# Performance work log

Measured on AMD Instinct MI355X. Metric: run time of the kernel, lower is better.

Reference implementation:

```python
import jax, jax.numpy as jnp
import numpy as np

B, S, E, H = 2, 2048, 1024, 16
D = E // H  # head dim = 64


def setup_inputs() -> dict:
    key = jax.random.key(0)
    ks = jax.random.split(key, 6)
    x = jax.random.normal(ks[0], (B, S, E), dtype=jnp.float32)
    attn_mask = jax.random.bernoulli(ks[1], 0.1, (B, S, S))  # True = masked
    scale = 1.0 / np.sqrt(E)
    w_kernel = jax.random.normal(ks[2], (E, 3 * E), dtype=jnp.float32) * scale
    w_bias = jax.random.normal(ks[3], (3 * E,), dtype=jnp.float32) * 0.02
    fc_kernel = jax.random.normal(ks[4], (E, E), dtype=jnp.float32) * scale
    fc_bias = jax.random.normal(ks[5], (E,), dtype=jnp.float32) * 0.02
    return {"x": x, "attn_mask": attn_mask, "w_kernel": w_kernel,
            "w_bias": w_bias, "fc_kernel": fc_kernel, "fc_bias": fc_bias}


def reference(x, attn_mask, w_kernel, w_bias, fc_kernel, fc_bias):
    b, s, e = x.shape
    qkv = jnp.einsum("bse,ef->bsf", x, w_kernel) + w_bias  # (B,S,3E)
    q, k, v = jnp.split(qkv, 3, axis=-1)

    def heads(t):  # (B,S,E) -> (B,H,S,D)
        return t.reshape(b, s, H, D).transpose(0, 2, 1, 3)

    q, k, v = heads(q), heads(k), heads(v)
    scores = jnp.einsum("bhqd,bhkd->bhqk", q, k) / jnp.sqrt(jnp.float32(D))
    # faithful quirk: masked positions are filled with 1e-9, not -inf
    scores = jnp.where(attn_mask[:, None, :, :], jnp.float32(1e-9), scores)
    A = jax.nn.softmax(scores, axis=-1)
    out = jnp.einsum("bhqk,bhkd->bhqd", A, v)  # (B,H,S,D)
    out = out.transpose(0, 2, 1, 3).reshape(b, s, e)
    # dropout is identity in eval mode
    return jnp.einsum("bse,ef->bsf", out, fc_kernel) + fc_bias
```

## Files before the change

kernel.cpp:

```cpp
#include <hip/hip_runtime.h>
#include <math.h>

#define BB 2
#define SS 2048
#define EE 1024
#define HH 16

typedef _Float16 f16;
typedef __attribute__((ext_vector_type(8))) _Float16 f16x8;
typedef __attribute__((ext_vector_type(4))) _Float16 f16x4;
typedef __attribute__((ext_vector_type(2))) _Float16 f16x2;
typedef __attribute__((ext_vector_type(4))) float f32x4;

union P8 { f16x8 v8; f16x2 h2[4]; };
union V8 { f16x8 v8; f16x4 v4[2]; };

#define QSCALE 0.18033688011112042f

#if __has_builtin(__builtin_amdgcn_exp2f)
#define EXP2(x) __builtin_amdgcn_exp2f(x)
#else
#define EXP2(x) exp2f(x)
#endif

static __device__ __forceinline__ f16x2 pk2(float a, float b) {
#if __has_builtin(__builtin_amdgcn_cvt_pkrtz)
  return __builtin_bit_cast(f16x2, __builtin_amdgcn_cvt_pkrtz(a, b));
#else
  f16x2 r; r[0] = (f16)a; r[1] = (f16)b; return r;
#endif
}

static __device__ __forceinline__ void gl16(const void* g, void* l) {
  __builtin_amdgcn_global_load_lds(
      (const __attribute__((address_space(1))) void*)g,
      (__attribute__((address_space(3))) void*)l, 16, 0, 0);
}

__global__ __launch_bounds__(256) void cvt_f32_f16(
    const float* __restrict__ in, f16* __restrict__ out, int n)
{
  int i = (blockIdx.x * 256 + threadIdx.x) * 8;
  if (i >= n) return;
  float4 a = *(const float4*)(in + i);
  float4 b = *(const float4*)(in + i + 4);
  f16x8 o;
  o[0] = (f16)a.x; o[1] = (f16)a.y; o[2] = (f16)a.z; o[3] = (f16)a.w;
  o[4] = (f16)b.x; o[5] = (f16)b.y; o[6] = (f16)b.z; o[7] = (f16)b.w;
  *(f16x8*)(out + i) = o;
}

__global__ __launch_bounds__(256) void transpose_cvt(
    const float* __restrict__ in, f16* __restrict__ out, int K, int N)
{
  __shared__ float T[64][65];
  const int k0 = blockIdx.y * 64, n0 = blockIdx.x * 64;
  const int tr = threadIdx.x >> 4, tc = (threadIdx.x & 15) * 4;
#pragma unroll
  for (int i = 0; i < 4; ++i) {
    int r = tr + i * 16;
    *(float4*)&T[r][tc] = *(const float4*)(in + (size_t)(k0 + r) * N + n0 + tc);
  }
  __syncthreads();
#pragma unroll
  for (int i = 0; i < 4; ++i) {
    int nl = tr + i * 16;
    f16x4 v;
    v[0] = (f16)T[tc + 0][nl];
    v[1] = (f16)T[tc + 1][nl];
    v[2] = (f16)T[tc + 2][nl];
    v[3] = (f16)T[tc + 3][nl];
    *(f16x4*)(out + (size_t)(n0 + nl) * K + k0 + tc) = v;
  }
}

__global__ __launch_bounds__(256) void pack_mask(
    const int* __restrict__ m, unsigned long long* __restrict__ bits)
{
  const int i = blockIdx.x * 256 + threadIdx.x;
  const unsigned long long bal = __ballot(m[i] != 0);
  if ((threadIdx.x & 63) == 0) bits[i >> 6] = bal;
}

__global__ __launch_bounds__(256) void gemm_f16(
    const f16* __restrict__ A, const f16* __restrict__ Bt,
    const float* __restrict__ bias, int M, int N, int K, int mode,
    f16* __restrict__ oQK, f16* __restrict__ oVT, float* __restrict__ oF32)
{
  __shared__ f16 Ah[128 * 32];
  __shared__ f16 Bh[128 * 32];

  const int t = threadIdx.x;
  const int l = t & 63, w = t >> 6;
  const int l15 = l & 15, l4 = l >> 4;
  const int wr = w >> 1, wc = w & 1;
  const int n0 = blockIdx.x * 128, m0 = blockIdx.y * 128;

  const int srow = l >> 2;
  const int gch  = (l & 3) ^ (srow & 3);
  const f16* Ap0 = A + (size_t)(m0 + w * 32 + srow) * K + gch * 8;
  const f16* Ap1 = Ap0 + (size_t)16 * K;
  const f16* Bp0 = Bt + (size_t)(n0 + w * 32 + srow) * K + gch * 8;
  const f16* Bp1 = Bp0 + (size_t)16 * K;
  f16* ldsA0 = &Ah[(w * 32) * 32];
  f16* ldsA1 = &Ah[(w * 32 + 16) * 32];
  f16* ldsB0 = &Bh[(w * 32) * 32];
  f16* ldsB1 = &Bh[(w * 32 + 16) * 32];

  f32x4 acc[4][4] = {};
  const int csw = (l15 & 3);

  for (int k0 = 0; k0 < K; k0 += 32) {
    gl16(Ap0 + k0, ldsA0);
    gl16(Ap1 + k0, ldsA1);
    gl16(Bp0 + k0, ldsB0);
    gl16(Bp1 + k0, ldsB1);
    __syncthreads();

    f16x8 af[4], bf[4];
#pragma unroll
    for (int mr = 0; mr < 4; ++mr) {
      const int row = wr * 64 + mr * 16 + l15;
      af[mr] = *(const f16x8*)&Ah[row * 32 + ((l4 ^ csw) * 8)];
    }
#pragma unroll
    for (int nr = 0; nr < 4; ++nr) {
      const int row = wc * 64 + nr * 16 + l15;
      bf[nr] = *(const f16x8*)&Bh[row * 32 + ((l4 ^ csw) * 8)];
    }
    __builtin_amdgcn_s_setprio(1);
#pragma unroll
    for (int mr = 0; mr < 4; ++mr)
#pragma unroll
      for (int nr = 0; nr < 4; ++nr)
        acc[mr][nr] = __builtin_amdgcn_mfma_f32_16x16x32_f16(
            af[mr], bf[nr], acc[mr][nr], 0, 0, 0);
    __builtin_amdgcn_s_setprio(0);
    __syncthreads();
  }

  if (mode == 1) {
#pragma unroll
    for (int nr = 0; nr < 4; ++nr) {
      const int n = n0 + wc * 64 + nr * 16 + l15;
      const float bv = bias[n];
#pragma unroll
      for (int mr = 0; mr < 4; ++mr)
#pragma unroll
        for (int j = 0; j < 4; ++j) {
          const int m = m0 + wr * 64 + mr * 16 + l4 * 4 + j;
          oF32[(size_t)m * N + n] = acc[mr][nr][j] + bv;
        }
    }
  } else {
#pragma unroll
    for (int nr = 0; nr < 4; ++nr) {
      const int n = n0 + wc * 64 + nr * 16 + l15;
      const float bv = bias[n];
      if (n < 2048) {
        const float qs = (n < 1024) ? QSCALE : 1.0f;
#pragma unroll
        for (int mr = 0; mr < 4; ++mr)
#pragma unroll
          for (int j = 0; j < 4; ++j) {
            const int m = m0 + wr * 64 + mr * 16 + l4 * 4 + j;
            oQK[(size_t)m * 2048 + n] = (f16)((acc[mr][nr][j] + bv) * qs);
          }
      } else {
        const int hh = (n - 2048) >> 6;
        const int d = (n - 2048) & 63;
#pragma unroll
        for (int mr = 0; mr < 4; ++mr) {
          const int tok0 = m0 + wr * 64 + mr * 16 + l4 * 4;
          const int bq = tok0 >> 11, sq = tok0 & 2047;
          f16x4 v;
          v[0] = (f16)(acc[mr][nr][0] + bv);
          v[1] = (f16)(acc[mr][nr][1] + bv);
          v[2] = (f16)(acc[mr][nr][2] + bv);
          v[3] = (f16)(acc[mr][nr][3] + bv);
          *(f16x4*)(oVT + ((size_t)(bq * 16 + hh) * 64 + d) * SS + sq) = v;
        }
      }
    }
  }
}

#define VPAD 36
__global__ __launch_bounds__(256, 4) void attn_mfma(
    const f16* __restrict__ qkbuf, const f16* __restrict__ vT,
    const unsigned long long* __restrict__ mbits,
    f16* __restrict__ Opart, float* __restrict__ Lpart)
{
  __shared__ f16 Kds[2][32 * 64];
  __shared__ f16 Vds[2][64 * VPAD];

  const int t = threadIdx.x;
  const int w = t >> 6, l = t & 63, l15 = l & 15, l4 = l >> 4;
  const int bh = blockIdx.y, b = bh >> 4, h = bh & 15;
  const int ks = blockIdx.z;
  const int qbase = blockIdx.x * 128 + w * 32;

  f16x8 q00, q01, q10, q11;
  {
    const size_t r0 = (size_t)(b * SS + qbase + l15) * 2048 + h * 64;
    const size_t r1 = (size_t)(b * SS + qbase + 16 + l15) * 2048 + h * 64;
    q00 = *(const f16x8*)(qkbuf + r0 + l4 * 8);
    q01 = *(const f16x8*)(qkbuf + r0 + 32 + l4 * 8);
    q10 = *(const f16x8*)(qkbuf + r1 + l4 * 8);
    q11 = *(const f16x8*)(qkbuf + r1 + 32 + l4 * 8);
  }

  f32x4 accA[4] = {}, accB[4] = {};
  f32x4 accLA = {}, accLB = {};
  f16x8 ones;
#pragma unroll
  for (int i = 0; i < 8; ++i) ones[i] = (f16)1.0f;

  const unsigned int* mA =
      (const unsigned int*)mbits + (size_t)(b * SS + qbase + l15) * 64 + ks * 32;
  const unsigned int* mB =
      (const unsigned int*)mbits + (size_t)(b * SS + qbase + 16 + l15) * 64 + ks * 32;

  const int srow = t >> 3;
  const int scb  = (t & 7) * 8;
  const int sws  = (srow & 7) << 3;
  const f16* kb = qkbuf + (size_t)b * SS * 2048 + 1024 + h * 64 + scb +
                  (size_t)ks * 1024 * 2048;
  const int vd  = t >> 2;
  const int vkb = (t & 3) * 8;
  const f16* vb = vT + ((size_t)bh * 64 + vd) * SS + ks * 1024 + vkb;

  f16x8 kr0; V8 vr0;
#define LOADT(kt)                                                         \
  {                                                                       \
    kr0 = *(const f16x8*)(kb + (size_t)((kt) + srow) * 2048);             \
    vr0.v8 = *(const f16x8*)(vb + (kt));                                  \
  }
#define COMMIT(bi)                                                        \
  {                                                                       \
    *(f16x8*)&Kds[bi][srow * 64 + (scb ^ sws)] = kr0;                     \
    *(f16x4*)&Vds[bi][vd * VPAD + vkb]     = vr0.v4[0];                   \
    *(f16x4*)&Vds[bi][vd * VPAD + vkb + 4] = vr0.v4[1];                   \
  }

  LOADT(0)
  COMMIT(0)
  LOADT(32)
  __syncthreads();

  const int swr = (l15 & 7) << 3;

#define BODY(cur, tI)                                                         \
  {                                                                           \
    const unsigned int mbA = mA[tI];                                          \
    const unsigned int mbB = mB[tI];                                          \
    float pA[8], pB[8];                                                       \
    _Pragma("unroll")                                                         \
    for (int g = 0; g < 2; ++g) {                                             \
      const f16* krow = &Kds[cur][(g * 16 + l15) * 64];                       \
      const f16x8 k0 = *(const f16x8*)(krow + ((l4 * 8) ^ swr));              \
      const f16x8 k1 = *(const f16x8*)(krow + ((32 + l4 * 8) ^ swr));         \
      __builtin_amdgcn_s_setprio(1);                                          \
      f32x4 SA = __builtin_amdgcn_mfma_f32_16x16x32_f16(                      \
          k0, q00, (f32x4){0.f, 0.f, 0.f, 0.f}, 0, 0, 0);                     \
      SA = __builtin_amdgcn_mfma_f32_16x16x32_f16(k1, q01, SA, 0, 0, 0);      \
      f32x4 SB = __builtin_amdgcn_mfma_f32_16x16x32_f16(                      \
          k0, q10, (f32x4){0.f, 0.f, 0.f, 0.f}, 0, 0, 0);                     \
      SB = __builtin_amdgcn_mfma_f32_16x16x32_f16(k1, q11, SB, 0, 0, 0);      \
      __builtin_amdgcn_s_setprio(0);                                          \
      const unsigned int nibA = mbA >> (g * 16 + l4 * 4);                     \
      const unsigned int nibB = mbB >> (g * 16 + l4 * 4);                     \
      _Pragma("unroll")                                                       \
      for (int j = 0; j < 4; ++j) {                                           \
        pA[g * 4 + j] = ((nibA >> j) & 1u) ? 1.0f : EXP2(SA[j]);              \
        pB[g * 4 + j] = ((nibB >> j) & 1u) ? 1.0f : EXP2(SB[j]);              \
      }                                                                       \
    }                                                                         \
    P8 uA, uB;                                                                \
    uA.h2[0] = pk2(pA[0], pA[1]); uA.h2[1] = pk2(pA[2], pA[3]);               \
    uA.h2[2] = pk2(pA[4], pA[5]); uA.h2[3] = pk2(pA[6], pA[7]);               \
    uB.h2[0] = pk2(pB[0], pB[1]); uB.h2[1] = pk2(pB[2], pB[3]);               \
    uB.h2[2] = pk2(pB[4], pB[5]); uB.h2[3] = pk2(pB[6], pB[7]);               \
    __builtin_amdgcn_s_setprio(1);                                            \
    _Pragma("unroll")                                                         \
    for (int dg = 0; dg < 4; ++dg) {                                          \
      const f16* vrow = &Vds[cur][(dg * 16 + l15) * VPAD];                    \
      V8 uv;                                                                  \
      uv.v4[0] = *(const f16x4*)(vrow + l4 * 4);                              \
      uv.v4[1] = *(const f16x4*)(vrow + 16 + l4 * 4);                         \
      accA[dg] = __builtin_amdgcn_mfma_f32_16x16x32_f16(uA.v8, uv.v8,         \
                                                        accA[dg], 0, 0, 0);   \
      accB[dg] = __builtin_amdgcn_mfma_f32_16x16x32_f16(uB.v8, uv.v8,         \
                                                        accB[dg], 0, 0, 0);   \
    }                                                                         \
    accLA = __builtin_amdgcn_mfma_f32_16x16x32_f16(uA.v8, ones, accLA,        \
                                                   0, 0, 0);                  \
    accLB = __builtin_amdgcn_mfma_f32_16x16x32_f16(uB.v8, ones, accLB,        \
                                                   0, 0, 0);                  \
    __builtin_amdgcn_s_setprio(0);                                            \
    if ((tI) + 1 < 32) {                                                      \
      COMMIT((cur) ^ 1)                                                       \
      if ((tI) + 2 < 32) LOADT(((tI) + 2) * 32)                               \
    }                                                                         \
    __syncthreads();                                                          \
  }

  for (int tI = 0; tI < 32; tI += 2) {
    BODY(0, tI)
    BODY(1, tI + 1)
  }

  const size_t obase = (size_t)ks * 4096 * EE;
#pragma unroll
  for (int j = 0; j < 4; ++j) {
    const int qr = l4 * 4 + j;
    const size_t rowA = (size_t)(b * SS + qbase + qr) * EE + h * 64 + l15;
    const size_t rowB = (size_t)(b * SS + qbase + 16 + qr) * EE + h * 64 + l15;
#pragma unroll
    for (int dg = 0; dg < 4; ++dg) {
      Opart[obase + rowA + dg * 16] = (f16)accA[dg][j];
      Opart[obase + rowB + dg * 16] = (f16)accB[dg][j];
    }
    if (l15 == 0) {
      Lpart[(size_t)ks * 4096 * HH + (size_t)(b * SS + qbase + qr) * HH + h] =
          accLA[j];
      Lpart[(size_t)ks * 4096 * HH +
            (size_t)(b * SS + qbase + 16 + qr) * HH + h] = accLB[j];
    }
  }
}

__global__ __launch_bounds__(256) void combine(
    const f16* __restrict__ Opart, const float* __restrict__ Lpart,
    f16* __restrict__ aout)
{
  const size_t i = ((size_t)blockIdx.x * 256 + threadIdx.x) * 8;
  const int token = (int)(i >> 10);
  const int h = (int)((i >> 6) & 15);
  const float inv =
      1.0f / (Lpart[(size_t)token * HH + h] +
              Lpart[(size_t)4096 * HH + (size_t)token * HH + h]);
  const f16x8 o0 = *(const f16x8*)(Opart + i);
  const f16x8 o1 = *(const f16x8*)(Opart + (size_t)4096 * EE + i);
  f16x8 o;
#pragma unroll
  for (int j = 0; j < 8; ++j)
    o[j] = (f16)(((float)o0[j] + (float)o1[j]) * inv);
  *(f16x8*)(aout + i) = o;
}

extern "C" void kernel_launch(void* const* d_in, const int* in_sizes, int n_in,
                              void* d_out, int out_size, void* d_ws,
                              size_t ws_size, hipStream_t stream)
{
  (void)in_sizes; (void)n_in; (void)out_size; (void)ws_size;
  const float* x   = (const float*)d_in[0];
  const int* mask  = (const int*)d_in[1];
  const float* wk  = (const float*)d_in[2];
  const float* wb  = (const float*)d_in[3];
  const float* fck = (const float*)d_in[4];
  const float* fcb = (const float*)d_in[5];
  float* out       = (float*)d_out;

  char* ws = (char*)d_ws;
  f16* fckT = (f16*)(ws);
  f16* qk   = (f16*)(ws + 2097152);
  f16* vT   = (f16*)(ws + 18874368);
  unsigned long long* mbits = (unsigned long long*)(ws + 27262976);
  float* Lp = (float*)(ws + 28311552);
  char* scratch = ws + 28835840;
  f16* xh    = (f16*)scratch;
  f16* Wt    = (f16*)(scratch + 8388608);
  f16* Opart = (f16*)scratch;
  f16* aoutH = qk;

  cvt_f32_f16<<<4096 * 1024 / (8 * 256), 256, 0, stream>>>(x, xh, 4096 * 1024);
  transpose_cvt<<<dim3(3072 / 64, 1024 / 64), 256, 0, stream>>>(wk, Wt, 1024, 3072);
  transpose_cvt<<<dim3(1024 / 64, 1024 / 64), 256, 0, stream>>>(fck, fckT, 1024, 1024);
  pack_mask<<<BB * SS * SS / 256, 256, 0, stream>>>(mask, mbits);

  gemm_f16<<<dim3(3072 / 128, 4096 / 128), 256, 0, stream>>>(
      xh, Wt, wb, 4096, 3072, 1024, 0, qk, vT, nullptr);

  attn_mfma<<<dim3(SS / 128, BB * HH, 2), 256, 0, stream>>>(
      qk, vT, mbits, Opart, Lp);
  combine<<<4096 * 1024 / (8 * 256), 256, 0, stream>>>(Opart, Lp, aoutH);

  gemm_f16<<<dim3(1024 / 128, 4096 / 128), 256, 0, stream>>>(
      aoutH, fckT, fcb, 4096, 1024, 1024, 1, nullptr, nullptr, out);
}
```

Before: 243.3 us.

## Merge prep kernels, stage QK epilogue through LDS, retile FC GEMM

Folds the four preprocessing kernels (x conversion, two weight transposes, mask packing) into a single launch that splits the work by block index, removing three launches. The QKV GEMM is specialised and its Q/K epilogue now goes through swizzled shared memory so each row is written with wide 16-byte stores instead of scattered 2-byte ones. The output-projection GEMM uses 128x64 tiles to double the block count and improve occupancy on the smaller N=1024 problem. The extra LDS round-trip and syncs add some epilogue cost.

```diff
diff --git a/kernel.cpp b/kernel.cpp
--- a/kernel.cpp
+++ b/kernel.cpp
@@ -37,58 +37,75 @@
       (__attribute__((address_space(3))) void*)l, 16, 0, 0);
 }
 
-__global__ __launch_bounds__(256) void cvt_f32_f16(
-    const float* __restrict__ in, f16* __restrict__ out, int n)
-{
-  int i = (blockIdx.x * 256 + threadIdx.x) * 8;
-  if (i >= n) return;
-  float4 a = *(const float4*)(in + i);
-  float4 b = *(const float4*)(in + i + 4);
-  f16x8 o;
-  o[0] = (f16)a.x; o[1] = (f16)a.y; o[2] = (f16)a.z; o[3] = (f16)a.w;
-  o[4] = (f16)b.x; o[5] = (f16)b.y; o[6] = (f16)b.z; o[7] = (f16)b.w;
-  *(f16x8*)(out + i) = o;
-}
-
-__global__ __launch_bounds__(256) void transpose_cvt(
-    const float* __restrict__ in, f16* __restrict__ out, int K, int N)
-{
+__global__ __launch_bounds__(256) void prep(
+    const float* __restrict__ x, f16* __restrict__ xh,
+    const float* __restrict__ wk, f16* __restrict__ Wt,
+    const float* __restrict__ fck, f16* __restrict__ fckT,
+    const int* __restrict__ mask, unsigned long long* __restrict__ mbits)
+{
+  const int bid = blockIdx.x;
+  const int tid = threadIdx.x;
   __shared__ float T[64][65];
-  const int k0 = blockIdx.y * 64, n0 = blockIdx.x * 64;
-  const int tr = threadIdx.x >> 4, tc = (threadIdx.x & 15) * 4;
-#pragma unroll
-  for (int i = 0; i < 4; ++i) {
-    int r = tr + i * 16;
-    *(float4*)&T[r][tc] = *(const float4*)(in + (size_t)(k0 + r) * N + n0 + tc);
-  }
-  __syncthreads();
-#pragma unroll
-  for (int i = 0; i < 4; ++i) {
-    int nl = tr + i * 16;
-    f16x4 v;
-    v[0] = (f16)T[tc + 0][nl];
-    v[1] = (f16)T[tc + 1][nl];
-    v[2] = (f16)T[tc + 2][nl];
-    v[3] = (f16)T[tc + 3][nl];
-    *(f16x4*)(out + (size_t)(n0 + nl) * K + k0 + tc) = v;
-  }
-}
-
-__global__ __launch_bounds__(256) void pack_mask(
-    const int* __restrict__ m, unsigned long long* __restrict__ bits)
-{
-  const int i = blockIdx.x * 256 + threadIdx.x;
-  const unsigned long long bal = __ballot(m[i] != 0);
-  if ((threadIdx.x & 63) == 0) bits[i >> 6] = bal;
-}
-
-__global__ __launch_bounds__(256) void gemm_f16(
+
+  if (bid < 2048) {
+    const int i = (bid * 256 + tid) * 8;
+    float4 a = *(const float4*)(x + i);
+    float4 b = *(const float4*)(x + i + 4);
+    f16x8 o;
+    o[0] = (f16)a.x; o[1] = (f16)a.y; o[2] = (f16)a.z; o[3] = (f16)a.w;
+    o[4] = (f16)b.x; o[5] = (f16)b.y; o[6] = (f16)b.z; o[7] = (f16)b.w;
+    *(f16x8*)(xh + i) = o;
+    return;
+  }
+  if (bid < 3072) {
+    const float* in; f16* outp; int K, N, bx, by;
+    if (bid < 2816) {
+      const int lb = bid - 2048;
+      bx = lb % 48; by = lb / 48; in = wk; outp = Wt; K = 1024; N = 3072;
+    } else {
+      const int lb = bid - 2816;
+      bx = lb & 15; by = lb >> 4; in = fck; outp = fckT; K = 1024; N = 1024;
+    }
+    const int k0 = by * 64, n0 = bx * 64;
+    const int tr = tid >> 4, tc = (tid & 15) * 4;
+#pragma unroll
+    for (int i = 0; i < 4; ++i) {
+      int r = tr + i * 16;
+      *(float4*)&T[r][tc] = *(const float4*)(in + (size_t)(k0 + r) * N + n0 + tc);
+    }
+    __syncthreads();
+#pragma unroll
+    for (int i = 0; i < 4; ++i) {
+      int nl = tr + i * 16;
+      f16x4 v;
+      v[0] = (f16)T[tc + 0][nl];
+      v[1] = (f16)T[tc + 1][nl];
+      v[2] = (f16)T[tc + 2][nl];
+      v[3] = (f16)T[tc + 3][nl];
+      *(f16x4*)(outp + (size_t)(n0 + nl) * K + k0 + tc) = v;
+    }
+    return;
+  }
+  const int lb = bid - 3072;
+  const int wg = lb * 4 + (tid >> 6);
+  const int lane = tid & 63;
+  const size_t base = (size_t)wg * 256;
+#pragma unroll
+  for (int k = 0; k < 4; ++k) {
+    const unsigned long long bal = __ballot(mask[base + k * 64 + lane] != 0);
+    if (lane == 0) mbits[(base >> 6) + k] = bal;
+  }
+}
+
+__global__ __launch_bounds__(256) void gemm_qkv(
     const f16* __restrict__ A, const f16* __restrict__ Bt,
-    const float* __restrict__ bias, int M, int N, int K, int mode,
-    f16* __restrict__ oQK, f16* __restrict__ oVT, float* __restrict__ oF32)
-{
-  __shared__ f16 Ah[128 * 32];
-  __shared__ f16 Bh[128 * 32];
+    const float* __restrict__ bias,
+    f16* __restrict__ oQK, f16* __restrict__ oVT)
+{
+  __shared__ f16 SH[8192];
+  f16* Ah = SH;
+  f16* Bh = SH + 4096;
+  const int K = 1024;
 
   const int t = threadIdx.x;
   const int l = t & 63, w = t >> 6;
@@ -139,49 +156,123 @@
     __syncthreads();
   }
 
-  if (mode == 1) {
+  if (n0 < 2048) {
+    const float qs = (n0 < 1024) ? QSCALE : 1.0f;
+#pragma unroll
+    for (int half = 0; half < 2; ++half) {
+      __syncthreads();
+      if (wr == half) {
+#pragma unroll
+        for (int nr = 0; nr < 4; ++nr) {
+          const int col = wc * 64 + nr * 16 + l15;
+          const float bv = bias[n0 + col];
+#pragma unroll
+          for (int mr = 0; mr < 4; ++mr)
+#pragma unroll
+            for (int j = 0; j < 4; ++j) {
+              const int r = mr * 16 + l4 * 4 + j;
+              SH[r * 128 + ((((col >> 3) ^ (r & 15)) << 3) | (col & 7))] =
+                  (f16)((acc[mr][nr][j] + bv) * qs);
+            }
+        }
+      }
+      __syncthreads();
+#pragma unroll
+      for (int cc = 0; cc < 4; ++cc) {
+        const int row = w * 16 + cc * 4 + (l >> 4);
+        const int ch  = l & 15;
+        const f16x8 v =
+            *(const f16x8*)&SH[row * 128 + ((ch ^ (row & 15)) << 3)];
+        *(f16x8*)(oQK + (size_t)(m0 + half * 64 + row) * 2048 + n0 + ch * 8) = v;
+      }
+    }
+  } else {
 #pragma unroll
     for (int nr = 0; nr < 4; ++nr) {
       const int n = n0 + wc * 64 + nr * 16 + l15;
       const float bv = bias[n];
-#pragma unroll
-      for (int mr = 0; mr < 4; ++mr)
-#pragma unroll
-        for (int j = 0; j < 4; ++j) {
-          const int m = m0 + wr * 64 + mr * 16 + l4 * 4 + j;
-          oF32[(size_t)m * N + n] = acc[mr][nr][j] + bv;
-        }
-    }
-  } else {
-#pragma unroll
-    for (int nr = 0; nr < 4; ++nr) {
-      const int n = n0 + wc * 64 + nr * 16 + l15;
-      const float bv = bias[n];
-      if (n < 2048) {
-        const float qs = (n < 1024) ? QSCALE : 1.0f;
-#pragma unroll
-        for (int mr = 0; mr < 4; ++mr)
-#pragma unroll
-          for (int j = 0; j < 4; ++j) {
-            const int m = m0 + wr * 64 + mr * 16 + l4 * 4 + j;
-            oQK[(size_t)m * 2048 + n] = (f16)((acc[mr][nr][j] + bv) * qs);
-          }
-      } else {
-        const int hh = (n - 2048) >> 6;
-        const int d = (n - 2048) & 63;
-#pragma unroll
-        for (int mr = 0; mr < 4; ++mr) {
-          const int tok0 = m0 + wr * 64 + mr * 16 + l4 * 4;
-          const int bq = tok0 >> 11, sq = tok0 & 2047;
-          f16x4 v;
-          v[0] = (f16)(acc[mr][nr][0] + bv);
-          v[1] = (f16)(acc[mr][nr][1] + bv);
-          v[2] = (f16)(acc[mr][nr][2] + bv);
-          v[3] = (f16)(acc[mr][nr][3] + bv);
-          *(f16x4*)(oVT + ((size_t)(bq * 16 + hh) * 64 + d) * SS + sq) = v;
-        }
+      const int hh = (n - 2048) >> 6;
+      const int d = (n - 2048) & 63;
+#pragma unroll
+      for (int mr = 0; mr < 4; ++mr) {
+        const int tok0 = m0 + wr * 64 + mr * 16 + l4 * 4;
+        const int bq = tok0 >> 11, sq = tok0 & 2047;
+        f16x4 v;
+        v[0] = (f16)(acc[mr][nr][0] + bv);
+        v[1] = (f16)(acc[mr][nr][1] + bv);
+        v[2] = (f16)(acc[mr][nr][2] + bv);
+        v[3] = (f16)(acc[mr][nr][3] + bv);
+        *(f16x4*)(oVT + ((size_t)(bq * 16 + hh) * 64 + d) * SS + sq) = v;
       }
     }
+  }
+}
+
+__global__ __launch_bounds__(256) void gemm_fc(
+    const f16* __restrict__ A, const f16* __restrict__ Bt,
+    const float* __restrict__ bias, float* __restrict__ outF)
+{
+  __shared__ f16 Ah[128 * 32];
+  __shared__ f16 Bh[64 * 32];
+  const int K = 1024, N = 1024;
+
+  const int t = threadIdx.x;
+  const int l = t & 63, w = t >> 6;
+  const int l15 = l & 15, l4 = l >> 4;
+  const int wr = w >> 1, wc = w & 1;
+  const int n0 = blockIdx.x * 64, m0 = blockIdx.y * 128;
+
+  const int srow = l >> 2;
+  const int gch  = (l & 3) ^ (srow & 3);
+  const f16* Ap0 = A + (size_t)(m0 + w * 32 + srow) * K + gch * 8;
+  const f16* Ap1 = Ap0 + (size_t)16 * K;
+  const f16* Bp0 = Bt + (size_t)(n0 + w * 16 + srow) * K + gch * 8;
+  f16* ldsA0 = &Ah[(w * 32) * 32];
+  f16* ldsA1 = &Ah[(w * 32 + 16) * 32];
+  f16* ldsB0 = &Bh[(w * 16) * 32];
+
+  f32x4 acc[4][2] = {};
+  const int csw = (l15 & 3);
+
+  for (int k0 = 0; k0 < K; k0 += 32) {
+    gl16(Ap0 + k0, ldsA0);
+    gl16(Ap1 + k0, ldsA1);
+    gl16(Bp0 + k0, ldsB0);
+    __syncthreads();
+
+    f16x8 af[4], bf[2];
+#pragma unroll
+    for (int mr = 0; mr < 4; ++mr) {
+      const int row = wr * 64 + mr * 16 + l15;
+      af[mr] = *(const f16x8*)&Ah[row * 32 + ((l4 ^ csw) * 8)];
+    }
+#pragma unroll
+    for (int nr = 0; nr < 2; ++nr) {
+      const int row = wc * 32 + nr * 16 + l15;
+      bf[nr] = *(const f16x8*)&Bh[row * 32 + ((l4 ^ csw) * 8)];
+    }
+    __builtin_amdgcn_s_setprio(1);
+#pragma unroll
+    for (int mr = 0; mr < 4; ++mr)
+#pragma unroll
+      for (int nr = 0; nr < 2; ++nr)
+        acc[mr][nr] = __builtin_amdgcn_mfma_f32_16x16x32_f16(
+            af[mr], bf[nr], acc[mr][nr], 0, 0, 0);
+    __builtin_amdgcn_s_setprio(0);
+    __syncthreads();
+  }
+
+#pragma unroll
+  for (int nr = 0; nr < 2; ++nr) {
+    const int n = n0 + wc * 32 + nr * 16 + l15;
+    const float bv = bias[n];
+#pragma unroll
+    for (int mr = 0; mr < 4; ++mr)
+#pragma unroll
+      for (int j = 0; j < 4; ++j) {
+        const int m = m0 + wr * 64 + mr * 16 + l4 * 4 + j;
+        outF[(size_t)m * N + n] = acc[mr][nr][j] + bv;
+      }
   }
 }
 
@@ -374,18 +465,15 @@
   f16* Opart = (f16*)scratch;
   f16* aoutH = qk;
 
-  cvt_f32_f16<<<4096 * 1024 / (8 * 256), 256, 0, stream>>>(x, xh, 4096 * 1024);
-  transpose_cvt<<<dim3(3072 / 64, 1024 / 64), 256, 0, stream>>>(wk, Wt, 1024, 3072);
-  transpose_cvt<<<dim3(1024 / 64, 1024 / 64), 256, 0, stream>>>(fck, fckT, 1024, 1024);
-  pack_mask<<<BB * SS * SS / 256, 256, 0, stream>>>(mask, mbits);
-
-  gemm_f16<<<dim3(3072 / 128, 4096 / 128), 256, 0, stream>>>(
-      xh, Wt, wb, 4096, 3072, 1024, 0, qk, vT, nullptr);
+  prep<<<11264, 256, 0, stream>>>(x, xh, wk, Wt, fck, fckT, mask, mbits);
+
+  gemm_qkv<<<dim3(3072 / 128, 4096 / 128), 256, 0, stream>>>(
+      xh, Wt, wb, qk, vT);
 
   attn_mfma<<<dim3(SS / 128, BB * HH, 2), 256, 0, stream>>>(
       qk, vT, mbits, Opart, Lp);
   combine<<<4096 * 1024 / (8 * 256), 256, 0, stream>>>(Opart, Lp, aoutH);
 
-  gemm_f16<<<dim3(1024 / 128, 4096 / 128), 256, 0, stream>>>(
-      aoutH, fckT, fcb, 4096, 1024, 1024, 1, nullptr, nullptr, out);
-}
+  gemm_fc<<<dim3(1024 / 64, 4096 / 128), 256, 0, stream>>>(
+      aoutH, fckT, fcb, out);
+}
```

Result: faster. 237.5 us (-2.4%).
